# Kernel optimization log

Hardware: AMD Instinct MI355X
Metric: run time of the kernel (lower is better)

The kernel has to match this reference:

```python
import jax, jax.numpy as jnp
import numpy as np

BATCH, C_IN, C_OUT, H, K = 32, 128, 256, 56, 3

def setup_inputs() -> dict:
    key = jax.random.key(0)
    k1, k2 = jax.random.split(key)
    img = jax.random.normal(k1, (BATCH, C_IN, H, H), dtype=jnp.float32)
    # matches nn.Parameter((rand - 0.5) * (1 / (C_IN * K**2)))
    filtro = (jax.random.uniform(k2, (C_OUT, C_IN, K, K), dtype=jnp.float32) - 0.5) * (1.0 / (C_IN * K * K))
    return {"img": img, "filtro": filtro}

def reference(img, filtro):
    # Original: padding=0 (stride=1), im2col unfold + matmul == VALID cross-correlation.
    return jax.lax.conv_general_dilated(
        img, filtro,
        window_strides=(1, 1),
        padding="VALID",
        dimension_numbers=("NCHW", "OIHW", "NCHW"),
    )  # -> [BATCH, C_OUT, H-K+1, H-K+1]
```

## Files before the change

### kernel.cpp

```cpp
#include <hip/hip_runtime.h>


#define BB   32
#define CIN  128
#define COUT 256
#define HH   56
#define WW   56
#define OH   54
#define OW   54

typedef short bf16x8 __attribute__((ext_vector_type(8)));
typedef float f32x4  __attribute__((ext_vector_type(4)));
typedef unsigned short u16x8 __attribute__((ext_vector_type(8)));

#define GLOAD_LDS16(g, l) __builtin_amdgcn_global_load_lds( \
    (const __attribute__((address_space(1))) unsigned int*)(g), \
    (__attribute__((address_space(3))) unsigned int*)(l), 16, 0, 0)

static __device__ __forceinline__ unsigned short f2bf(float f) {
    unsigned int u = __float_as_uint(f);
    u += 0x7FFFu + ((u >> 16) & 1u);
    return (unsigned short)(u >> 16);
}

__global__ __launch_bounds__(256) void prep_all(const float* __restrict__ img,
                                                const float* __restrict__ flt,
                                                unsigned short* __restrict__ imgT,
                                                unsigned short* __restrict__ filtG) {
    if (blockIdx.x < BB * HH) {
        const int b = blockIdx.x / HH;
        const int y = blockIdx.x - b * HH;
        for (int i = threadIdx.x; i < 16 * WW; i += 256) {
            const int g = i / WW;
            const int x = i - g * WW;
            unsigned short pk[8];
            #pragma unroll
            for (int j = 0; j < 8; ++j)
                pk[j] = f2bf(img[((size_t)(b * CIN + g * 8 + j) * HH + y) * WW + x]);
            *(u16x8*)(imgT + ((size_t)(b * HH + y) * WW + x) * CIN + g * 8) = *(u16x8*)pk;
        }
    } else {
        const int idx = (blockIdx.x - BB * HH) * 256 + threadIdx.x;
        const int co = idx >> 7;
        const int ci = idx & 127;
        const int cot = co >> 7, col = co & 127;
        const int c = ci >> 5, kg = (ci >> 3) & 3, e = ci & 7;
        const size_t base = (size_t)(cot * 4 + c) * 36864 + kg * 1024 + col * 8 + e;
        #pragma unroll
        for (int t = 0; t < 9; ++t)
            filtG[base + t * 4096] = f2bf(flt[(size_t)(co * CIN + ci) * 9 + t]);
    }
}

#define IMG_ROWB  896
#define IMG_PLANE 8960
#define IMG_BUF   35840
#define FLTA_OFF  71680
#define FLTB_OFF  112640
#define LDS_BYTES 145408

template<int T0, int NT>
static __device__ __forceinline__ void compute_taps(const char* __restrict__ aR,
                                                    const char* __restrict__ bBc,
                                                    f32x4 (&acc)[4][7]) {
    #pragma unroll
    for (int tt = 0; tt < NT; ++tt) {
        const int t = T0 + tt;
        const int dy = t / 3, dx = t % 3;
        bf16x8 A[4];
        #pragma unroll
        for (int cf = 0; cf < 4; ++cf)
            A[cf] = *(const bf16x8*)(aR + tt * 8192 + cf * 256);
        #pragma unroll
        for (int xo = 0; xo < 7; ++xo) {
            bf16x8 bv = *(const bf16x8*)(bBc + dy * IMG_ROWB + (xo * 8 + dx) * 16);
            #pragma unroll
            for (int cf = 0; cf < 4; ++cf)
                acc[cf][xo] = __builtin_amdgcn_mfma_f32_16x16x32_bf16(A[cf], bv, acc[cf][xo], 0, 0, 0);
        }
    }
}

__global__ __launch_bounds__(512, 1) void conv_mfma(
    const unsigned short* __restrict__ imgT,
    const unsigned short* __restrict__ filtG,
    float* __restrict__ out)
{
    __shared__ char lds[LDS_BYTES];

    const int tid  = threadIdx.x;
    const int lane = tid & 63, w8 = tid >> 6;
    const int ch   = w8 >> 2, rp = w8 & 3;
    const int sub  = lane & 15, kg = lane >> 4;
    const int sr   = sub >> 3,  sc = sub & 7;

    const int w    = (blockIdx.x & 7) * 56 + (blockIdx.x >> 3);
    const int cot  = w & 1;
    const int rest = w >> 1;
    const int strip = rest % 7;
    const int b     = rest / 7;
    const int co0   = cot * 128;
    const int ystart = (strip < 6) ? strip * 8 : (OH - 8);

    char* const pImg = lds;
    char* const pFA  = lds + FLTA_OFF;
    char* const pFB  = lds + FLTB_OFF;
    const char* bB = pImg + kg * IMG_PLANE + (rp * 2 + sr) * IMG_ROWB + sc * 16;
    const char* aA = pFA + kg * 2048 + (ch * 64 + sub) * 16;
    const char* aB = pFB + kg * 2048 + (ch * 64 + sub) * 16;

    const unsigned short* fsrc = filtG + (size_t)cot * 147456;

    const int hs = tid >> 8, t8 = tid & 255;
    int goffI[3];
    #pragma unroll
    for (int k = 0; k < 3; ++k) {
        const int s = k * 256 + t8;
        const int r = s / 56;
        const int x = s - r * 56;
        goffI[k] = ((b * HH + ystart + r) * WW + x) * CIN + hs * 8;
    }
    const bool act2 = (t8 < 48);

    #define STAGE_FA(cn) do { \
        _Pragma("unroll") \
        for (int k = 0; k < 5; ++k) \
            GLOAD_LDS16(fsrc + (cn) * 36864 + (k * 512 + tid) * 8, \
                        pFA + (k * 512 + tid) * 16); \
    } while (0)
    #define STAGE_FB(cn) do { \
        _Pragma("unroll") \
        for (int k = 0; k < 4; ++k) \
            GLOAD_LDS16(fsrc + (cn) * 36864 + 20480 + (k * 512 + tid) * 8, \
                        pFB + (k * 512 + tid) * 16); \
    } while (0)
    #define STAGE_I01(cn) do { \
        char* d_ = pImg + ((cn) & 1) * IMG_BUF + hs * IMG_PLANE; \
        _Pragma("unroll") \
        for (int k = 0; k < 3; ++k) \
            if (k < 2 || act2) \
                GLOAD_LDS16(imgT + goffI[k] + (cn) * 32, d_ + (k * 256 + t8) * 16); \
    } while (0)
    #define STAGE_I23(cn) do { \
        char* d_ = pImg + ((cn) & 1) * IMG_BUF + (2 + hs) * IMG_PLANE; \
        _Pragma("unroll") \
        for (int k = 0; k < 3; ++k) \
            if (k < 2 || act2) \
                GLOAD_LDS16(imgT + goffI[k] + (cn) * 32 + 16, d_ + (k * 256 + t8) * 16); \
    } while (0)
    #define PHASE_SYNC() do { \
        asm volatile("s_waitcnt vmcnt(0) lgkmcnt(0)" ::: "memory"); \
        __builtin_amdgcn_s_barrier(); \
        __builtin_amdgcn_sched_barrier(0); \
    } while (0)

    f32x4 acc[4][7];
    #pragma unroll
    for (int cf = 0; cf < 4; ++cf)
        #pragma unroll
        for (int xo = 0; xo < 7; ++xo) acc[cf][xo] = (f32x4)0.0f;

    STAGE_FA(0);
    STAGE_I01(0);
    STAGE_I23(0);
    PHASE_SYNC();

    #define CONV_ITER(C) do { \
         \
        STAGE_FB(C); \
        if ((C) < 3) STAGE_I01((C) + 1); \
        { const char* bBc = bB + ((C) & 1) * IMG_BUF; \
          __builtin_amdgcn_s_setprio(1); \
          compute_taps<0, 5>(aA, bBc, acc); \
          __builtin_amdgcn_s_setprio(0); } \
        PHASE_SYNC(); \
         \
        if ((C) < 3) { STAGE_FA((C) + 1); STAGE_I23((C) + 1); } \
        { const char* bBc = bB + ((C) & 1) * IMG_BUF; \
          __builtin_amdgcn_s_setprio(1); \
          compute_taps<5, 4>(aB, bBc, acc); \
          __builtin_amdgcn_s_setprio(0); } \
        if ((C) < 3) PHASE_SYNC(); \
    } while (0)

    CONV_ITER(0);
    CONV_ITER(1);
    CONV_ITER(2);
    CONV_ITER(3);

    const int y = ystart + rp * 2 + sr;
    #pragma unroll
    for (int cf = 0; cf < 4; ++cf) {
        const int cob = co0 + ch * 64 + cf * 16 + kg * 4;
        #pragma unroll
        for (int xo = 0; xo < 7; ++xo) {
            const int x = xo * 8 + sc;
            if (x < OW) {
                float* o = out + ((size_t)(b * COUT + cob) * OH + y) * OW + x;
                #pragma unroll
                for (int j = 0; j < 4; ++j)
                    o[(size_t)j * OH * OW] = acc[cf][xo][j];
            }
        }
    }
}

#define COB  16
#define THF  6
#define CIBF 2
#define IRF  (THF + 2)
__global__ __launch_bounds__(256) void conv3x3_fp32(
    const float* __restrict__ img, const float* __restrict__ flt,
    float* __restrict__ out)
{
    __shared__ float si[CIBF][IRF][WW];
    __shared__ float sf[CIBF][COB][9];
    const int tid = threadIdx.x;
    const int tx  = tid & 63;
    const int tg  = tid >> 6;
    int bid = blockIdx.x;
    const int ytile = bid % (OH / THF);  bid /= (OH / THF);
    const int cob   = bid % (COUT / COB); bid /= (COUT / COB);
    const int b     = bid;
    const int y0  = ytile * THF;
    const int co0 = cob * COB;
    float acc[4][THF];
    #pragma unroll
    for (int c = 0; c < 4; ++c)
        #pragma unroll
        for (int y = 0; y < THF; ++y) acc[c][y] = 0.0f;
    for (int ci0 = 0; ci0 < CIN; ci0 += CIBF) {
        for (int i = tid; i < CIBF * IRF * (WW / 4); i += 256) {
            const int cil = i / (IRF * (WW / 4));
            int rem = i - cil * (IRF * (WW / 4));
            const int r = rem / (WW / 4);
            const int v = rem - r * (WW / 4);
            const float4* src = reinterpret_cast<const float4*>(
                img + (((size_t)b * CIN + (ci0 + cil)) * HH + (y0 + r)) * WW) + v;
            reinterpret_cast<float4*>(&si[cil][r][0])[v] = *src;
        }
        for (int i = tid; i < CIBF * COB * 9; i += 256) {
            const int cil = i / (COB * 9);
            int rem = i - cil * (COB * 9);
            const int col = rem / 9;
            const int e   = rem - col * 9;
            sf[cil][col][e] = flt[(((size_t)(co0 + col)) * CIN + (ci0 + cil)) * 9 + e];
        }
        __syncthreads();
        if (tx < OW) {
            #pragma unroll
            for (int cil = 0; cil < CIBF; ++cil) {
                float f[4][9];
                #pragma unroll
                for (int c = 0; c < 4; ++c)
                    #pragma unroll
                    for (int e = 0; e < 9; ++e) f[c][e] = sf[cil][tg * 4 + c][e];
                float a[IRF][3];
                #pragma unroll
                for (int r = 0; r < IRF; ++r) {
                    a[r][0] = si[cil][r][tx + 0];
                    a[r][1] = si[cil][r][tx + 1];
                    a[r][2] = si[cil][r][tx + 2];
                }
                #pragma unroll
                for (int y = 0; y < THF; ++y)
                    #pragma unroll
                    for (int dy = 0; dy < 3; ++dy)
                        #pragma unroll
                        for (int c = 0; c < 4; ++c)
                            acc[c][y] = fmaf(a[y + dy][0], f[c][dy * 3 + 0],
                                        fmaf(a[y + dy][1], f[c][dy * 3 + 1],
                                        fmaf(a[y + dy][2], f[c][dy * 3 + 2], acc[c][y])));
            }
        }
        __syncthreads();
    }
    if (tx < OW) {
        #pragma unroll
        for (int c = 0; c < 4; ++c) {
            const int co = co0 + tg * 4 + c;
            #pragma unroll
            for (int y = 0; y < THF; ++y)
                out[(((size_t)b * COUT + co) * OH + (y0 + y)) * OW + tx] = acc[c][y];
        }
    }
}

extern "C" void kernel_launch(void* const* d_in, const int* in_sizes, int n_in,
                              void* d_out, int out_size, void* d_ws, size_t ws_size,
                              hipStream_t stream) {
    const float* img = (const float*)d_in[0];
    const float* flt = (const float*)d_in[1];
    float* out = (float*)d_out;

    const size_t IMGT_BYTES = (size_t)BB * HH * WW * CIN * 2;
    const size_t FILT_BYTES = (size_t)2 * 4 * 36864 * 2;
    if (ws_size < IMGT_BYTES + FILT_BYTES) {
        conv3x3_fp32<<<BB * (COUT / COB) * (OH / THF), 256, 0, stream>>>(img, flt, out);
        return;
    }
    unsigned short* imgT  = (unsigned short*)d_ws;
    unsigned short* filtG = (unsigned short*)((char*)d_ws + IMGT_BYTES);

    prep_all<<<BB * HH + 128, 256, 0, stream>>>(img, flt, imgT, filtG);
    conv_mfma<<<2 * 7 * BB, 512, 0, stream>>>(imgT, filtG, out);
}
```

Measured before the change: 93.33 us.

## Split conv blocks to 64 output channels with register-pipelined LDS tap reads

Each block now handles 64 output channels with 4 waves instead of 128 channels with 8 waves. This halves the LDS footprint, so two blocks can share a CU. The image double buffer is replaced by a single buffer, so staging now waits on barriers. Per-tap LDS reads are issued through inline ds_read_b128 into double-buffered registers, with lgkmcnt waits so the next tap's reads overlap the current tap's MFMAs. The trade-off is that the image tile is fetched twice as often across blocks, and global loads no longer overlap compute within a block except through the second resident block.

```diff
diff --git a/kernel.cpp b/kernel.cpp
--- a/kernel.cpp
+++ b/kernel.cpp
@@ -17,6 +17,8 @@
     (const __attribute__((address_space(1))) unsigned int*)(g), \
     (__attribute__((address_space(3))) unsigned int*)(l), 16, 0, 0)
 
+#define LDS_ADDR(p) ((unsigned)(size_t)(__attribute__((address_space(3))) char*)(p))
+
 static __device__ __forceinline__ unsigned short f2bf(float f) {
     unsigned int u = __float_as_uint(f);
     u += 0x7FFFu + ((u >> 16) & 1u);
@@ -26,7 +28,7 @@
 __global__ __launch_bounds__(256) void prep_all(const float* __restrict__ img,
                                                 const float* __restrict__ flt,
                                                 unsigned short* __restrict__ imgT,
-                                                unsigned short* __restrict__ filtG) {
+                                                unsigned short* __restrict__ filtP) {
     if (blockIdx.x < BB * HH) {
         const int b = blockIdx.x / HH;
         const int y = blockIdx.x - b * HH;
@@ -43,155 +45,163 @@
         const int idx = (blockIdx.x - BB * HH) * 256 + threadIdx.x;
         const int co = idx >> 7;
         const int ci = idx & 127;
-        const int cot = co >> 7, col = co & 127;
+        const int cot = co >> 6, col = co & 63;
         const int c = ci >> 5, kg = (ci >> 3) & 3, e = ci & 7;
-        const size_t base = (size_t)(cot * 4 + c) * 36864 + kg * 1024 + col * 8 + e;
+        const size_t base = (size_t)(cot * 4 + c) * 18432 + kg * 512 + col * 8 + e;
         #pragma unroll
         for (int t = 0; t < 9; ++t)
-            filtG[base + t * 4096] = f2bf(flt[(size_t)(co * CIN + ci) * 9 + t]);
+            filtP[base + t * 2048] = f2bf(flt[(size_t)(co * CIN + ci) * 9 + t]);
     }
 }
 
 #define IMG_ROWB  896
 #define IMG_PLANE 8960
-#define IMG_BUF   35840
-#define FLTA_OFF  71680
-#define FLTB_OFF  112640
-#define LDS_BYTES 145408
-
-template<int T0, int NT>
-static __device__ __forceinline__ void compute_taps(const char* __restrict__ aR,
-                                                    const char* __restrict__ bBc,
-                                                    f32x4 (&acc)[4][7]) {
-    #pragma unroll
-    for (int tt = 0; tt < NT; ++tt) {
-        const int t = T0 + tt;
-        const int dy = t / 3, dx = t % 3;
-        bf16x8 A[4];
+#define FLTA_OFF  35840
+#define FLTB_OFF  56320
+#define LDS_BYTES 72704
+
+template<int PAR, int S, int DY, int DX>
+static __device__ __forceinline__ void rd_tap(unsigned ab, unsigned bb,
+                                              bf16x8 (&fAr)[2][4],
+                                              bf16x8 (&fBr)[2][7]) {
+    #pragma unroll
+    for (int cf = 0; cf < 4; ++cf)
+        asm volatile("ds_read_b128 %0, %1 offset:%c2"
+                     : "=v"(fAr[PAR][cf]) : "v"(ab), "i"(S * 4096 + cf * 256));
+    #pragma unroll
+    for (int xo = 0; xo < 7; ++xo)
+        asm volatile("ds_read_b128 %0, %1 offset:%c2"
+                     : "=v"(fBr[PAR][xo]) : "v"(bb), "i"(DY * 896 + (xo * 8 + DX) * 16));
+}
+
+template<int PAR>
+static __device__ __forceinline__ void mfma_tap(const bf16x8 (&fAr)[2][4],
+                                                const bf16x8 (&fBr)[2][7],
+                                                f32x4 (&acc)[4][7]) {
+    __builtin_amdgcn_s_setprio(1);
+    #pragma unroll
+    for (int xo = 0; xo < 7; ++xo)
         #pragma unroll
         for (int cf = 0; cf < 4; ++cf)
-            A[cf] = *(const bf16x8*)(aR + tt * 8192 + cf * 256);
-        #pragma unroll
-        for (int xo = 0; xo < 7; ++xo) {
-            bf16x8 bv = *(const bf16x8*)(bBc + dy * IMG_ROWB + (xo * 8 + dx) * 16);
-            #pragma unroll
-            for (int cf = 0; cf < 4; ++cf)
-                acc[cf][xo] = __builtin_amdgcn_mfma_f32_16x16x32_bf16(A[cf], bv, acc[cf][xo], 0, 0, 0);
-        }
-    }
-}
-
-__global__ __launch_bounds__(512, 1) void conv_mfma(
+            acc[cf][xo] = __builtin_amdgcn_mfma_f32_16x16x32_bf16(
+                fAr[PAR][cf], fBr[PAR][xo], acc[cf][xo], 0, 0, 0);
+    __builtin_amdgcn_s_setprio(0);
+}
+
+#define WAITK11 do { asm volatile("s_waitcnt lgkmcnt(11)" ::: "memory"); \
+                     __builtin_amdgcn_sched_barrier(0); } while (0)
+#define WAITK0  do { asm volatile("s_waitcnt lgkmcnt(0)" ::: "memory"); \
+                     __builtin_amdgcn_sched_barrier(0); } while (0)
+#define BARRIER do { __builtin_amdgcn_s_barrier(); \
+                     __builtin_amdgcn_sched_barrier(0); } while (0)
+#define DRAIN_BAR do { asm volatile("s_waitcnt vmcnt(0) lgkmcnt(0)" ::: "memory"); \
+                       __builtin_amdgcn_s_barrier(); \
+                       __builtin_amdgcn_sched_barrier(0); } while (0)
+
+__global__ __launch_bounds__(256, 2) void conv_mfma(
     const unsigned short* __restrict__ imgT,
-    const unsigned short* __restrict__ filtG,
+    const unsigned short* __restrict__ filtP,
     float* __restrict__ out)
 {
     __shared__ char lds[LDS_BYTES];
 
     const int tid  = threadIdx.x;
-    const int lane = tid & 63, w8 = tid >> 6;
-    const int ch   = w8 >> 2, rp = w8 & 3;
+    const int lane = tid & 63, rp = tid >> 6;
     const int sub  = lane & 15, kg = lane >> 4;
     const int sr   = sub >> 3,  sc = sub & 7;
 
-    const int w    = (blockIdx.x & 7) * 56 + (blockIdx.x >> 3);
-    const int cot  = w & 1;
-    const int rest = w >> 1;
+    const int w    = (blockIdx.x & 7) * 112 + (blockIdx.x >> 3);
+    const int cot  = w & 3;
+    const int rest = w >> 2;
     const int strip = rest % 7;
     const int b     = rest / 7;
-    const int co0   = cot * 128;
+    const int co0   = cot * 64;
     const int ystart = (strip < 6) ? strip * 8 : (OH - 8);
 
     char* const pImg = lds;
     char* const pFA  = lds + FLTA_OFF;
     char* const pFB  = lds + FLTB_OFF;
-    const char* bB = pImg + kg * IMG_PLANE + (rp * 2 + sr) * IMG_ROWB + sc * 16;
-    const char* aA = pFA + kg * 2048 + (ch * 64 + sub) * 16;
-    const char* aB = pFB + kg * 2048 + (ch * 64 + sub) * 16;
-
-    const unsigned short* fsrc = filtG + (size_t)cot * 147456;
-
-    const int hs = tid >> 8, t8 = tid & 255;
-    int goffI[3];
-    #pragma unroll
-    for (int k = 0; k < 3; ++k) {
-        const int s = k * 256 + t8;
-        const int r = s / 56;
-        const int x = s - r * 56;
-        goffI[k] = ((b * HH + ystart + r) * WW + x) * CIN + hs * 8;
-    }
-    const bool act2 = (t8 < 48);
-
+
+    const unsigned bbv = LDS_ADDR(pImg + kg * IMG_PLANE + (2 * rp + sr) * IMG_ROWB + sc * 16);
+    const unsigned aab = LDS_ADDR(pFA + kg * 1024 + sub * 16);
+    const unsigned abb = LDS_ADDR(pFB + kg * 1024 + sub * 16);
+
+    const unsigned short* fsrc = filtP + (size_t)cot * 73728;
+
+    int goff[9];
+    #pragma unroll
+    for (int k = 0; k < 9; ++k) {
+        const int s = k * 256 + tid;
+        const int plane = s / 560;
+        const int rem = s - plane * 560;
+        const int r = rem / 56;
+        const int x = rem - r * 56;
+        goff[k] = ((b * HH + ystart + r) * WW + x) * CIN + plane * 8;
+    }
+    const bool act8 = (tid < 192);
+    char* const iDst = pImg + tid * 16;
+    char* const aDst = pFA + tid * 16;
+    char* const bDst = pFB + tid * 16;
+
+    #define STAGE_IMG(cn) do { \
+        _Pragma("unroll") \
+        for (int k = 0; k < 9; ++k) \
+            if (k < 8 || act8) \
+                GLOAD_LDS16(imgT + goff[k] + (cn) * 32, iDst + k * 4096); \
+    } while (0)
     #define STAGE_FA(cn) do { \
         _Pragma("unroll") \
         for (int k = 0; k < 5; ++k) \
-            GLOAD_LDS16(fsrc + (cn) * 36864 + (k * 512 + tid) * 8, \
-                        pFA + (k * 512 + tid) * 16); \
+            GLOAD_LDS16(fsrc + (cn) * 18432 + (k * 256 + tid) * 8, aDst + k * 4096); \
     } while (0)
     #define STAGE_FB(cn) do { \
         _Pragma("unroll") \
         for (int k = 0; k < 4; ++k) \
-            GLOAD_LDS16(fsrc + (cn) * 36864 + 20480 + (k * 512 + tid) * 8, \
-                        pFB + (k * 512 + tid) * 16); \
+            GLOAD_LDS16(fsrc + (cn) * 18432 + 10240 + (k * 256 + tid) * 8, bDst + k * 4096); \
     } while (0)
-    #define STAGE_I01(cn) do { \
-        char* d_ = pImg + ((cn) & 1) * IMG_BUF + hs * IMG_PLANE; \
-        _Pragma("unroll") \
-        for (int k = 0; k < 3; ++k) \
-            if (k < 2 || act2) \
-                GLOAD_LDS16(imgT + goffI[k] + (cn) * 32, d_ + (k * 256 + t8) * 16); \
+
+    f32x4 acc[4][7];
+    #pragma unroll
+    for (int cf = 0; cf < 4; ++cf)
+        #pragma unroll
+        for (int xo = 0; xo < 7; ++xo) acc[cf][xo] = (f32x4)0.0f;
+
+    bf16x8 fAr[2][4], fBr[2][7];
+
+    STAGE_IMG(0);
+    STAGE_FA(0);
+    STAGE_FB(0);
+    DRAIN_BAR;
+
+    #define CITER(C) do { \
+        rd_tap<0, 0, 0, 0>(aab, bbv, fAr, fBr); \
+        rd_tap<1, 1, 0, 1>(aab, bbv, fAr, fBr); WAITK11; mfma_tap<0>(fAr, fBr, acc); \
+        rd_tap<0, 2, 0, 2>(aab, bbv, fAr, fBr); WAITK11; mfma_tap<1>(fAr, fBr, acc); \
+        rd_tap<1, 3, 1, 0>(aab, bbv, fAr, fBr); WAITK11; mfma_tap<0>(fAr, fBr, acc); \
+        rd_tap<0, 4, 1, 1>(aab, bbv, fAr, fBr); WAITK11; mfma_tap<1>(fAr, fBr, acc); \
+        WAITK0; mfma_tap<0>(fAr, fBr, acc); \
+        if ((C) < 3) { BARRIER; STAGE_FA((C) + 1); } \
+        rd_tap<1, 0, 1, 2>(abb, bbv, fAr, fBr); \
+        rd_tap<0, 1, 2, 0>(abb, bbv, fAr, fBr); WAITK11; mfma_tap<1>(fAr, fBr, acc); \
+        rd_tap<1, 2, 2, 1>(abb, bbv, fAr, fBr); WAITK11; mfma_tap<0>(fAr, fBr, acc); \
+        rd_tap<0, 3, 2, 2>(abb, bbv, fAr, fBr); WAITK11; mfma_tap<1>(fAr, fBr, acc); \
+        WAITK0; mfma_tap<0>(fAr, fBr, acc); \
+        if ((C) < 3) { \
+            BARRIER; \
+            STAGE_IMG((C) + 1); STAGE_FB((C) + 1); \
+            DRAIN_BAR; \
+        } \
     } while (0)
-    #define STAGE_I23(cn) do { \
-        char* d_ = pImg + ((cn) & 1) * IMG_BUF + (2 + hs) * IMG_PLANE; \
-        _Pragma("unroll") \
-        for (int k = 0; k < 3; ++k) \
-            if (k < 2 || act2) \
-                GLOAD_LDS16(imgT + goffI[k] + (cn) * 32 + 16, d_ + (k * 256 + t8) * 16); \
-    } while (0)
-    #define PHASE_SYNC() do { \
-        asm volatile("s_waitcnt vmcnt(0) lgkmcnt(0)" ::: "memory"); \
-        __builtin_amdgcn_s_barrier(); \
-        __builtin_amdgcn_sched_barrier(0); \
-    } while (0)
-
-    f32x4 acc[4][7];
-    #pragma unroll
-    for (int cf = 0; cf < 4; ++cf)
-        #pragma unroll
-        for (int xo = 0; xo < 7; ++xo) acc[cf][xo] = (f32x4)0.0f;
-
-    STAGE_FA(0);
-    STAGE_I01(0);
-    STAGE_I23(0);
-    PHASE_SYNC();
-
-    #define CONV_ITER(C) do { \
-         \
-        STAGE_FB(C); \
-        if ((C) < 3) STAGE_I01((C) + 1); \
-        { const char* bBc = bB + ((C) & 1) * IMG_BUF; \
-          __builtin_amdgcn_s_setprio(1); \
-          compute_taps<0, 5>(aA, bBc, acc); \
-          __builtin_amdgcn_s_setprio(0); } \
-        PHASE_SYNC(); \
-         \
-        if ((C) < 3) { STAGE_FA((C) + 1); STAGE_I23((C) + 1); } \
-        { const char* bBc = bB + ((C) & 1) * IMG_BUF; \
-          __builtin_amdgcn_s_setprio(1); \
-          compute_taps<5, 4>(aB, bBc, acc); \
-          __builtin_amdgcn_s_setprio(0); } \
-        if ((C) < 3) PHASE_SYNC(); \
-    } while (0)
-
-    CONV_ITER(0);
-    CONV_ITER(1);
-    CONV_ITER(2);
-    CONV_ITER(3);
-
-    const int y = ystart + rp * 2 + sr;
+
+    CITER(0);
+    CITER(1);
+    CITER(2);
+    CITER(3);
+
+    const int y = ystart + 2 * rp + sr;
     #pragma unroll
     for (int cf = 0; cf < 4; ++cf) {
-        const int cob = co0 + ch * 64 + cf * 16 + kg * 4;
+        const int cob = co0 + cf * 16 + kg * 4;
         #pragma unroll
         for (int xo = 0; xo < 7; ++xo) {
             const int x = xo * 8 + sc;
@@ -294,14 +304,14 @@
     float* out = (float*)d_out;
 
     const size_t IMGT_BYTES = (size_t)BB * HH * WW * CIN * 2;
-    const size_t FILT_BYTES = (size_t)2 * 4 * 36864 * 2;
+    const size_t FILT_BYTES = (size_t)4 * 73728 * 2;
     if (ws_size < IMGT_BYTES + FILT_BYTES) {
         conv3x3_fp32<<<BB * (COUT / COB) * (OH / THF), 256, 0, stream>>>(img, flt, out);
         return;
     }
     unsigned short* imgT  = (unsigned short*)d_ws;
-    unsigned short* filtG = (unsigned short*)((char*)d_ws + IMGT_BYTES);
-
-    prep_all<<<BB * HH + 128, 256, 0, stream>>>(img, flt, imgT, filtG);
-    conv_mfma<<<2 * 7 * BB, 512, 0, stream>>>(imgT, filtG, out);
-}
+    unsigned short* filtP = (unsigned short*)((char*)d_ws + IMGT_BYTES);
+
+    prep_all<<<BB * HH + 128, 256, 0, stream>>>(img, flt, imgT, filtP);
+    conv_mfma<<<4 * 7 * BB, 256, 0, stream>>>(imgT, filtP, out);
+}
```

After: 103.7 us. 11.2% more time.
